# Performance work log

Hardware: AMD Instinct MI355X
Metric: run time of the kernel (lower is better)

The kernel has to match this reference:

```python
import jax, jax.numpy as jnp
import numpy as np

D_MODEL = 1024
D_FF = 4096
NUM_EXPERTS = 8
TOP_K = 2
LN_EPS = 1e-5


def setup_inputs() -> dict:
    key = jax.random.key(0)
    ks = jax.random.split(key, 8)
    B, S = 4, 2048
    x = jax.random.normal(ks[0], (B, S, D_MODEL), dtype=jnp.float32)
    router_w = jax.random.normal(ks[1], (D_MODEL, NUM_EXPERTS), dtype=jnp.float32) * (1.0 / np.sqrt(D_MODEL))
    router_b = jnp.zeros((NUM_EXPERTS,), dtype=jnp.float32)
    w1 = jax.random.normal(ks[2], (NUM_EXPERTS, D_MODEL, D_FF), dtype=jnp.float32) * (1.0 / np.sqrt(D_MODEL))
    b1 = jnp.zeros((NUM_EXPERTS, D_FF), dtype=jnp.float32)
    w2 = jax.random.normal(ks[3], (NUM_EXPERTS, D_FF, D_MODEL), dtype=jnp.float32) * (1.0 / np.sqrt(D_FF))
    b2 = jnp.zeros((NUM_EXPERTS, D_MODEL), dtype=jnp.float32)
    gamma = jnp.ones((D_MODEL,), dtype=jnp.float32)
    beta = jnp.zeros((D_MODEL,), dtype=jnp.float32)
    return {"x": x, "router_w": router_w, "router_b": router_b,
            "w1": w1, "b1": b1, "w2": w2, "b2": b2,
            "gamma": gamma, "beta": beta}


def reference(x, router_w, router_b, w1, b1, w2, b2, gamma, beta):
    B, S, D = x.shape
    E = w1.shape[0]
    xf = x.reshape(B * S, D)  # [T, D]

    # Router: linear -> softmax -> top-k (scores are softmax probs of selected experts)
    logits = xf @ router_w + router_b                     # [T, E]
    probs = jax.nn.softmax(logits, axis=-1)
    scores, idx = jax.lax.top_k(probs, TOP_K)             # [T, K]

    # Dense combine weights: comb[t, e] = sum_k scores[t,k] * (idx[t,k]==e)
    comb = (jax.nn.one_hot(idx, E, dtype=x.dtype) * scores[..., None]).sum(axis=1)  # [T, E]

    # Dispatch/compute/combine. comb is 0 for unrouted (token, expert) pairs,
    # so the weighted sum matches the gather/scatter loop in the original.
    out = jnp.zeros_like(xf)
    for e in range(E):  # fixed small expert count, structurally distinct weights
        h = jax.nn.gelu(xf @ w1[e] + b1[e])               # [T, D_FF]
        out = out + comb[:, e:e + 1] * (h @ w2[e] + b2[e])
    out = out.reshape(B, S, D)

    # residual + LayerNorm (dropout = 0.0)
    y = x + out
    mu = y.mean(axis=-1, keepdims=True)
    var = ((y - mu) ** 2).mean(axis=-1, keepdims=True)
    z = (y - mu) * jax.lax.rsqrt(var + LN_EPS) * gamma + beta

    # routing decision export (bool mask over experts, jit-friendly stand-in for a Python set)
    selected = comb.sum(axis=0) > 0
    return z, selected
```

## Files before the change

### kernel.cpp

```cpp
#include <hip/hip_runtime.h>


#define T_TOKENS 8192
#define DM 1024
#define DF 4096
#define NE 8

typedef unsigned short u16;
typedef short v8s __attribute__((ext_vector_type(8)));
typedef float v4f __attribute__((ext_vector_type(4)));

__device__ __forceinline__ u16 f2bf(float f) {
  unsigned u = __float_as_uint(f);
  u += 0x7FFFu + ((u >> 16) & 1u);
  return (u16)(u >> 16);
}

__device__ __forceinline__ void load16_lds(const u16* g, u16* lds) {
  __builtin_amdgcn_global_load_lds(
      (const __attribute__((address_space(1))) unsigned int*)g,
      (__attribute__((address_space(3))) unsigned int*)lds, 16, 0, 0);
}

__global__ __launch_bounds__(256) void cvt_x_kernel(const float* __restrict__ x,
                                                    u16* __restrict__ xb) {
  size_t i = ((size_t)blockIdx.x * 256 + threadIdx.x) * 8;
  float4 v0 = *(const float4*)(x + i);
  float4 v1 = *(const float4*)(x + i + 4);
  int4 o;
  o.x = (int)f2bf(v0.x) | ((int)f2bf(v0.y) << 16);
  o.y = (int)f2bf(v0.z) | ((int)f2bf(v0.w) << 16);
  o.z = (int)f2bf(v1.x) | ((int)f2bf(v1.y) << 16);
  o.w = (int)f2bf(v1.z) | ((int)f2bf(v1.w) << 16);
  *(int4*)(xb + i) = o;
}

__global__ __launch_bounds__(64) void router_kernel(
    const float* __restrict__ x, const float* __restrict__ rw,
    const float* __restrict__ rb, int* __restrict__ counts,
    int* __restrict__ list_token, int* __restrict__ epos,
    float* __restrict__ escore) {
  int t = blockIdx.x;
  int lane = threadIdx.x;
  const float* xr = x + (size_t)t * DM;
  float a[8] = {0.f, 0.f, 0.f, 0.f, 0.f, 0.f, 0.f, 0.f};
  for (int j = lane; j < DM; j += 64) {
    float xv = xr[j];
    const float4* r4 = (const float4*)(rw + (size_t)j * 8);
    float4 w0 = r4[0], w1 = r4[1];
    a[0] += xv * w0.x; a[1] += xv * w0.y; a[2] += xv * w0.z; a[3] += xv * w0.w;
    a[4] += xv * w1.x; a[5] += xv * w1.y; a[6] += xv * w1.z; a[7] += xv * w1.w;
  }
#pragma unroll
  for (int e = 0; e < 8; e++)
#pragma unroll
    for (int off = 32; off > 0; off >>= 1) a[e] += __shfl_down(a[e], off);
  if (lane == 0) {
    float l[8];
    float mx = -1e30f;
#pragma unroll
    for (int e = 0; e < 8; e++) { l[e] = a[e] + rb[e]; mx = fmaxf(mx, l[e]); }
    float sum = 0.f;
#pragma unroll
    for (int e = 0; e < 8; e++) { l[e] = __expf(l[e] - mx); sum += l[e]; }
    float inv = 1.f / sum;
    int i1 = 0; float p1 = -1.f;
#pragma unroll
    for (int e = 0; e < 8; e++) if (l[e] > p1) { p1 = l[e]; i1 = e; }
    int i2 = -1; float p2 = -1.f;
#pragma unroll
    for (int e = 0; e < 8; e++) if (e != i1 && l[e] > p2) { p2 = l[e]; i2 = e; }
    int pos1 = atomicAdd(&counts[i1], 1);
    int pos2 = atomicAdd(&counts[i2], 1);
    list_token[i1 * T_TOKENS + pos1] = t;
    list_token[i2 * T_TOKENS + pos2] = t;
    epos[2 * t] = (i1 << 16) | pos1;
    epos[2 * t + 1] = (i2 << 16) | pos2;
    escore[2 * t] = p1 * inv;
    escore[2 * t + 1] = p2 * inv;
  }
}

__global__ __launch_bounds__(64) void finalize_kernel(const int* __restrict__ counts,
                                                      int* __restrict__ offsets,
                                                      float* __restrict__ sel_out) {
  int tid = threadIdx.x;
  if (tid == 0) {
    int o = 0;
    for (int e = 0; e < NE; e++) { offsets[e] = o; o += counts[e]; }
    offsets[NE] = o;
  }
  if (tid < NE) sel_out[tid] = counts[tid] > 0 ? 1.f : 0.f;
}

__global__ __launch_bounds__(256) void transpose_cvt_kernel(
    const float* __restrict__ src, u16* __restrict__ dst, int R, int C) {
  __shared__ float tile[64][33];
  int e = blockIdx.z;
  const float* s = src + (size_t)e * R * C;
  u16* d = dst + (size_t)e * R * C;
  int c0 = blockIdx.x * 32, r0 = blockIdx.y * 64;
  int tx = threadIdx.x, ty = threadIdx.y;
#pragma unroll
  for (int i = 0; i < 8; i++) {
    int r = r0 + ty + i * 8;
    tile[ty + i * 8][tx] = s[(size_t)r * C + c0 + tx];
  }
  __syncthreads();
#pragma unroll
  for (int i = 0; i < 4; i++) {
    int c = c0 + ty + i * 8;
    unsigned lo = f2bf(tile[2 * tx][ty + i * 8]);
    unsigned hi = f2bf(tile[2 * tx + 1][ty + i * 8]);
    *(unsigned*)&d[(size_t)c * R + r0 + 2 * tx] = lo | (hi << 16);
  }
}

__global__ __launch_bounds__(256) void gemm1_kernel(
    const u16* __restrict__ xb, const u16* __restrict__ w1t,
    const float* __restrict__ b1, const int* __restrict__ counts,
    const int* __restrict__ offsets, const int* __restrict__ list_token,
    u16* __restrict__ H) {
  int e = blockIdx.z;
  int cnt = counts[e];
  int r0 = blockIdx.y * 128;
  if (r0 >= cnt) return;
  int n0 = blockIdx.x * 128;
  int rem = cnt - r0;

  __shared__ __align__(16) u16 As[128 * 32];
  __shared__ __align__(16) u16 Bs[128 * 32];

  int tid = threadIdx.x;
  int ra0 = tid >> 2, ca0 = tid & 3;
  int ra1 = ra0 + 64, ca1 = ca0;
  const int* lst = list_token + e * T_TOKENS + r0;
  int tok0 = (ra0 < rem) ? lst[ra0] : lst[0];
  int tok1 = (ra1 < rem) ? lst[ra1] : lst[0];
  const u16* gA0 = xb + (size_t)tok0 * DM + ca0 * 8;
  const u16* gA1 = xb + (size_t)tok1 * DM + ca1 * 8;
  const u16* gB0 = w1t + ((size_t)e * DF + n0 + ra0) * DM + ca0 * 8;
  const u16* gB1 = w1t + ((size_t)e * DF + n0 + ra1) * DM + ca1 * 8;

  int lane = tid & 63, wv = tid >> 6;
  u16* ldsA0 = As + wv * 512;
  u16* ldsA1 = As + 2048 + wv * 512;
  u16* ldsB0 = Bs + wv * 512;
  u16* ldsB1 = Bs + 2048 + wv * 512;

  int wm = (wv >> 1) * 64, wn = (wv & 1) * 64;
  int ml = lane & 15, quad = lane >> 4;

  v4f acc[4][4];
#pragma unroll
  for (int i = 0; i < 4; i++)
#pragma unroll
    for (int j = 0; j < 4; j++) acc[i][j] = (v4f){0.f, 0.f, 0.f, 0.f};

  for (int k0 = 0; k0 < DM; k0 += 32) {
    load16_lds(gA0 + k0, ldsA0);
    load16_lds(gA1 + k0, ldsA1);
    load16_lds(gB0 + k0, ldsB0);
    load16_lds(gB1 + k0, ldsB1);
    __syncthreads();
    v8s af[4], bf[4];
#pragma unroll
    for (int i = 0; i < 4; i++)
      af[i] = *(const v8s*)&As[(wm + i * 16 + ml) * 32 + quad * 8];
#pragma unroll
    for (int j = 0; j < 4; j++)
      bf[j] = *(const v8s*)&Bs[(wn + j * 16 + ml) * 32 + quad * 8];
#pragma unroll
    for (int i = 0; i < 4; i++)
#pragma unroll
      for (int j = 0; j < 4; j++)
        acc[i][j] = __builtin_amdgcn_mfma_f32_16x16x32_bf16(af[i], bf[j], acc[i][j], 0, 0, 0);
    __syncthreads();
  }

  int slotbase = offsets[e] + r0;
#pragma unroll
  for (int i = 0; i < 4; i++) {
    int rbase = wm + i * 16 + quad * 4;
#pragma unroll
    for (int j = 0; j < 4; j++) {
      int cc = n0 + wn + j * 16 + ml;
      float bias = b1[e * DF + cc];
#pragma unroll
      for (int r = 0; r < 4; r++) {
        int row = rbase + r;
        if (row < rem) {
          float v = acc[i][j][r] + bias;
          float u = 0.7978845608028654f * (v + 0.044715f * v * v * v);
          float h = v / (1.f + __expf(-2.f * u));
          H[(size_t)(slotbase + row) * DF + cc] = f2bf(h);
        }
      }
    }
  }
}

__global__ __launch_bounds__(256) void gemm2_kernel(
    const u16* __restrict__ H, const u16* __restrict__ w2t,
    const float* __restrict__ b2, const int* __restrict__ counts,
    const int* __restrict__ offsets, float* __restrict__ partial) {
  int e = blockIdx.z;
  int cnt = counts[e];
  int r0 = blockIdx.y * 128;
  if (r0 >= cnt) return;
  int n0 = blockIdx.x * 128;
  int rem = cnt - r0;
  int slotbase = offsets[e] + r0;

  __shared__ __align__(16) u16 As[128 * 32];
  __shared__ __align__(16) u16 Bs[128 * 32];

  int tid = threadIdx.x;
  int ra0 = tid >> 2, ca0 = tid & 3;
  int ra1 = ra0 + 64, ca1 = ca0;
  int ar0 = (ra0 < rem) ? ra0 : 0;
  int ar1 = (ra1 < rem) ? ra1 : 0;
  const u16* gA0 = H + (size_t)(slotbase + ar0) * DF + ca0 * 8;
  const u16* gA1 = H + (size_t)(slotbase + ar1) * DF + ca1 * 8;
  const u16* gB0 = w2t + ((size_t)e * DM + n0 + ra0) * DF + ca0 * 8;
  const u16* gB1 = w2t + ((size_t)e * DM + n0 + ra1) * DF + ca1 * 8;

  int lane = tid & 63, wv = tid >> 6;
  u16* ldsA0 = As + wv * 512;
  u16* ldsA1 = As + 2048 + wv * 512;
  u16* ldsB0 = Bs + wv * 512;
  u16* ldsB1 = Bs + 2048 + wv * 512;

  int wm = (wv >> 1) * 64, wn = (wv & 1) * 64;
  int ml = lane & 15, quad = lane >> 4;

  v4f acc[4][4];
#pragma unroll
  for (int i = 0; i < 4; i++)
#pragma unroll
    for (int j = 0; j < 4; j++) acc[i][j] = (v4f){0.f, 0.f, 0.f, 0.f};

  for (int k0 = 0; k0 < DF; k0 += 32) {
    load16_lds(gA0 + k0, ldsA0);
    load16_lds(gA1 + k0, ldsA1);
    load16_lds(gB0 + k0, ldsB0);
    load16_lds(gB1 + k0, ldsB1);
    __syncthreads();
    v8s af[4], bf[4];
#pragma unroll
    for (int i = 0; i < 4; i++)
      af[i] = *(const v8s*)&As[(wm + i * 16 + ml) * 32 + quad * 8];
#pragma unroll
    for (int j = 0; j < 4; j++)
      bf[j] = *(const v8s*)&Bs[(wn + j * 16 + ml) * 32 + quad * 8];
#pragma unroll
    for (int i = 0; i < 4; i++)
#pragma unroll
      for (int j = 0; j < 4; j++)
        acc[i][j] = __builtin_amdgcn_mfma_f32_16x16x32_bf16(af[i], bf[j], acc[i][j], 0, 0, 0);
    __syncthreads();
  }

#pragma unroll
  for (int i = 0; i < 4; i++) {
    int rbase = wm + i * 16 + quad * 4;
#pragma unroll
    for (int j = 0; j < 4; j++) {
      int cc = n0 + wn + j * 16 + ml;
      float bias = b2[e * DM + cc];
#pragma unroll
      for (int r = 0; r < 4; r++) {
        int row = rbase + r;
        if (row < rem)
          partial[(size_t)(slotbase + row) * DM + cc] = acc[i][j][r] + bias;
      }
    }
  }
}

__global__ __launch_bounds__(256) void ln_kernel(
    const float* __restrict__ x, const float* __restrict__ partial,
    const int* __restrict__ offsets, const int* __restrict__ epos,
    const float* __restrict__ escore, const float* __restrict__ gamma,
    const float* __restrict__ beta, float* __restrict__ out) {
  int t = blockIdx.x;
  int tid = threadIdx.x;
  int e0p = epos[2 * t], e1p = epos[2 * t + 1];
  float s0 = escore[2 * t], s1 = escore[2 * t + 1];
  size_t row0 = (size_t)offsets[e0p >> 16] + (e0p & 0xFFFF);
  size_t row1 = (size_t)offsets[e1p >> 16] + (e1p & 0xFFFF);
  float4 xv = ((const float4*)(x + (size_t)t * DM))[tid];
  float4 p0 = ((const float4*)(partial + row0 * DM))[tid];
  float4 p1 = ((const float4*)(partial + row1 * DM))[tid];
  float4 y;
  y.x = xv.x + s0 * p0.x + s1 * p1.x;
  y.y = xv.y + s0 * p0.y + s1 * p1.y;
  y.z = xv.z + s0 * p0.z + s1 * p1.z;
  y.w = xv.w + s0 * p0.w + s1 * p1.w;
  float s = y.x + y.y + y.z + y.w;
  float ss = y.x * y.x + y.y * y.y + y.z * y.z + y.w * y.w;
#pragma unroll
  for (int off = 32; off > 0; off >>= 1) {
    s += __shfl_down(s, off);
    ss += __shfl_down(ss, off);
  }
  __shared__ float red[10];
  int wid = tid >> 6, lane = tid & 63;
  if (lane == 0) { red[wid] = s; red[4 + wid] = ss; }
  __syncthreads();
  if (tid == 0) {
    float S = red[0] + red[1] + red[2] + red[3];
    float SS = red[4] + red[5] + red[6] + red[7];
    float mu = S * (1.f / DM);
    float var = SS * (1.f / DM) - mu * mu;
    red[8] = mu;
    red[9] = rsqrtf(var + 1e-5f);
  }
  __syncthreads();
  float mu = red[8], rs = red[9];
  float4 g = ((const float4*)gamma)[tid];
  float4 b = ((const float4*)beta)[tid];
  float4 z;
  z.x = (y.x - mu) * rs * g.x + b.x;
  z.y = (y.y - mu) * rs * g.y + b.y;
  z.z = (y.z - mu) * rs * g.z + b.z;
  z.w = (y.w - mu) * rs * g.w + b.w;
  ((float4*)(out + (size_t)t * DM))[tid] = z;
}

extern "C" void kernel_launch(void* const* d_in, const int* in_sizes, int n_in,
                              void* d_out, int out_size, void* d_ws, size_t ws_size,
                              hipStream_t stream) {
  const float* x = (const float*)d_in[0];
  const float* rw = (const float*)d_in[1];
  const float* rb = (const float*)d_in[2];
  const float* w1 = (const float*)d_in[3];
  const float* b1 = (const float*)d_in[4];
  const float* w2 = (const float*)d_in[5];
  const float* b2 = (const float*)d_in[6];
  const float* gamma = (const float*)d_in[7];
  const float* beta = (const float*)d_in[8];
  float* out = (float*)d_out;

  char* ws = (char*)d_ws;
  int* counts = (int*)(ws + 0);
  int* offsets = (int*)(ws + 256);
  int* list_token = (int*)(ws + 4096);
  int* epos = (int*)(ws + 266240);
  float* escore = (float*)(ws + 331776);
  u16* xb = (u16*)(ws + 1048576);
  u16* w1t = (u16*)(ws + 17825792);
  u16* w2t = (u16*)(ws + 84934656);
  u16* H = (u16*)(ws + 152043520);
  float* partial = (float*)(ws + 286261248);

  hipMemsetAsync(counts, 0, NE * sizeof(int), stream);

  cvt_x_kernel<<<dim3(4096), dim3(256), 0, stream>>>(x, xb);
  router_kernel<<<dim3(T_TOKENS), dim3(64), 0, stream>>>(x, rw, rb, counts,
                                                         list_token, epos, escore);
  finalize_kernel<<<dim3(1), dim3(64), 0, stream>>>(
      counts, offsets, out + (size_t)T_TOKENS * DM);
  transpose_cvt_kernel<<<dim3(128, 16, NE), dim3(32, 8), 0, stream>>>(w1, w1t, DM, DF);
  transpose_cvt_kernel<<<dim3(32, 64, NE), dim3(32, 8), 0, stream>>>(w2, w2t, DF, DM);

  gemm1_kernel<<<dim3(DF / 128, 64, NE), dim3(256), 0, stream>>>(
      xb, w1t, b1, counts, offsets, list_token, H);
  gemm2_kernel<<<dim3(DM / 128, 64, NE), dim3(256), 0, stream>>>(
      H, w2t, b2, counts, offsets, partial);
  ln_kernel<<<dim3(T_TOKENS), dim3(256), 0, stream>>>(x, partial, offsets, epos,
                                                      escore, gamma, beta, out);
}
```

Measured before the change: 1.034 ms.

## Fuse x conversion into router, widen transpose tiles, pack GELU output stores

Drops the separate x-to-bf16 kernel and has the router write the bf16 copy while it reads x, with the router now running four tokens per 256-thread block. The weight transpose-convert kernel moves to 64x64 tiles with float4 loads and 16-byte packed bf16 stores. gemm1's epilogue exchanges neighbouring columns through a lane shuffle so each even lane writes two bf16 values as one 32-bit store. These changes aim to cut launch overhead and memory transactions in the preprocessing and epilogue stages. The router's bf16 stores are 2-byte scalar writes, and the shuffle must now run on every lane, including rows past the valid count.

```diff
diff --git a/kernel.cpp b/kernel.cpp
--- a/kernel.cpp
+++ b/kernel.cpp
@@ -22,30 +22,19 @@
       (__attribute__((address_space(3))) unsigned int*)lds, 16, 0, 0);
 }
 
-__global__ __launch_bounds__(256) void cvt_x_kernel(const float* __restrict__ x,
-                                                    u16* __restrict__ xb) {
-  size_t i = ((size_t)blockIdx.x * 256 + threadIdx.x) * 8;
-  float4 v0 = *(const float4*)(x + i);
-  float4 v1 = *(const float4*)(x + i + 4);
-  int4 o;
-  o.x = (int)f2bf(v0.x) | ((int)f2bf(v0.y) << 16);
-  o.y = (int)f2bf(v0.z) | ((int)f2bf(v0.w) << 16);
-  o.z = (int)f2bf(v1.x) | ((int)f2bf(v1.y) << 16);
-  o.w = (int)f2bf(v1.z) | ((int)f2bf(v1.w) << 16);
-  *(int4*)(xb + i) = o;
-}
-
-__global__ __launch_bounds__(64) void router_kernel(
+__global__ __launch_bounds__(256) void router_kernel(
     const float* __restrict__ x, const float* __restrict__ rw,
     const float* __restrict__ rb, int* __restrict__ counts,
     int* __restrict__ list_token, int* __restrict__ epos,
-    float* __restrict__ escore) {
-  int t = blockIdx.x;
-  int lane = threadIdx.x;
+    float* __restrict__ escore, u16* __restrict__ xb) {
+  int w = threadIdx.x >> 6, lane = threadIdx.x & 63;
+  int t = blockIdx.x * 4 + w;
   const float* xr = x + (size_t)t * DM;
+  u16* xbr = xb + (size_t)t * DM;
   float a[8] = {0.f, 0.f, 0.f, 0.f, 0.f, 0.f, 0.f, 0.f};
   for (int j = lane; j < DM; j += 64) {
     float xv = xr[j];
+    xbr[j] = f2bf(xv);
     const float4* r4 = (const float4*)(rw + (size_t)j * 8);
     float4 w0 = r4[0], w1 = r4[1];
     a[0] += xv * w0.x; a[1] += xv * w0.y; a[2] += xv * w0.z; a[3] += xv * w0.w;
@@ -95,24 +84,36 @@
 
 __global__ __launch_bounds__(256) void transpose_cvt_kernel(
     const float* __restrict__ src, u16* __restrict__ dst, int R, int C) {
-  __shared__ float tile[64][33];
+  __shared__ float tile[64 * 65];
   int e = blockIdx.z;
   const float* s = src + (size_t)e * R * C;
   u16* d = dst + (size_t)e * R * C;
-  int c0 = blockIdx.x * 32, r0 = blockIdx.y * 64;
-  int tx = threadIdx.x, ty = threadIdx.y;
-#pragma unroll
-  for (int i = 0; i < 8; i++) {
-    int r = r0 + ty + i * 8;
-    tile[ty + i * 8][tx] = s[(size_t)r * C + c0 + tx];
+  int r0 = blockIdx.y * 64, c0 = blockIdx.x * 64;
+  int tid = threadIdx.x;
+  int pr = tid >> 4, pc4 = (tid & 15) * 4;
+#pragma unroll
+  for (int i = 0; i < 4; i++) {
+    int r = pr + i * 16;
+    float4 v = *(const float4*)(s + (size_t)(r0 + r) * C + c0 + pc4);
+    tile[r * 65 + pc4] = v.x;
+    tile[r * 65 + pc4 + 1] = v.y;
+    tile[r * 65 + pc4 + 2] = v.z;
+    tile[r * 65 + pc4 + 3] = v.w;
   }
   __syncthreads();
-#pragma unroll
-  for (int i = 0; i < 4; i++) {
-    int c = c0 + ty + i * 8;
-    unsigned lo = f2bf(tile[2 * tx][ty + i * 8]);
-    unsigned hi = f2bf(tile[2 * tx + 1][ty + i * 8]);
-    *(unsigned*)&d[(size_t)c * R + r0 + 2 * tx] = lo | (hi << 16);
+  int r8 = (tid & 7) * 8, cb = tid >> 3;
+#pragma unroll
+  for (int i = 0; i < 2; i++) {
+    int c = cb + i * 32;
+    unsigned pk0 = (unsigned)f2bf(tile[(r8 + 0) * 65 + c]) |
+                   ((unsigned)f2bf(tile[(r8 + 1) * 65 + c]) << 16);
+    unsigned pk1 = (unsigned)f2bf(tile[(r8 + 2) * 65 + c]) |
+                   ((unsigned)f2bf(tile[(r8 + 3) * 65 + c]) << 16);
+    unsigned pk2 = (unsigned)f2bf(tile[(r8 + 4) * 65 + c]) |
+                   ((unsigned)f2bf(tile[(r8 + 5) * 65 + c]) << 16);
+    unsigned pk3 = (unsigned)f2bf(tile[(r8 + 6) * 65 + c]) |
+                   ((unsigned)f2bf(tile[(r8 + 7) * 65 + c]) << 16);
+    *(uint4*)(d + (size_t)(c0 + c) * R + r0 + r8) = make_uint4(pk0, pk1, pk2, pk3);
   }
 }
 
@@ -133,14 +134,14 @@
 
   int tid = threadIdx.x;
   int ra0 = tid >> 2, ca0 = tid & 3;
-  int ra1 = ra0 + 64, ca1 = ca0;
+  int ra1 = ra0 + 64;
   const int* lst = list_token + e * T_TOKENS + r0;
   int tok0 = (ra0 < rem) ? lst[ra0] : lst[0];
   int tok1 = (ra1 < rem) ? lst[ra1] : lst[0];
   const u16* gA0 = xb + (size_t)tok0 * DM + ca0 * 8;
-  const u16* gA1 = xb + (size_t)tok1 * DM + ca1 * 8;
+  const u16* gA1 = xb + (size_t)tok1 * DM + ca0 * 8;
   const u16* gB0 = w1t + ((size_t)e * DF + n0 + ra0) * DM + ca0 * 8;
-  const u16* gB1 = w1t + ((size_t)e * DF + n0 + ra1) * DM + ca1 * 8;
+  const u16* gB1 = w1t + ((size_t)e * DF + n0 + ra1) * DM + ca0 * 8;
 
   int lane = tid & 63, wv = tid >> 6;
   u16* ldsA0 = As + wv * 512;
@@ -189,11 +190,13 @@
 #pragma unroll
       for (int r = 0; r < 4; r++) {
         int row = rbase + r;
-        if (row < rem) {
-          float v = acc[i][j][r] + bias;
-          float u = 0.7978845608028654f * (v + 0.044715f * v * v * v);
-          float h = v / (1.f + __expf(-2.f * u));
-          H[(size_t)(slotbase + row) * DF + cc] = f2bf(h);
+        float v = acc[i][j][r] + bias;
+        float u = 0.7978845608028654f * (v + 0.044715f * v * v * v);
+        float h = v / (1.f + __expf(-2.f * u));
+        float hp = __shfl_xor(h, 1);
+        if (((ml & 1) == 0) && row < rem) {
+          unsigned pk = (unsigned)f2bf(h) | ((unsigned)f2bf(hp) << 16);
+          *(unsigned*)&H[(size_t)(slotbase + row) * DF + cc] = pk;
         }
       }
     }
@@ -217,13 +220,13 @@
 
   int tid = threadIdx.x;
   int ra0 = tid >> 2, ca0 = tid & 3;
-  int ra1 = ra0 + 64, ca1 = ca0;
+  int ra1 = ra0 + 64;
   int ar0 = (ra0 < rem) ? ra0 : 0;
   int ar1 = (ra1 < rem) ? ra1 : 0;
   const u16* gA0 = H + (size_t)(slotbase + ar0) * DF + ca0 * 8;
-  const u16* gA1 = H + (size_t)(slotbase + ar1) * DF + ca1 * 8;
+  const u16* gA1 = H + (size_t)(slotbase + ar1) * DF + ca0 * 8;
   const u16* gB0 = w2t + ((size_t)e * DM + n0 + ra0) * DF + ca0 * 8;
-  const u16* gB1 = w2t + ((size_t)e * DM + n0 + ra1) * DF + ca1 * 8;
+  const u16* gB1 = w2t + ((size_t)e * DM + n0 + ra1) * DF + ca0 * 8;
 
   int lane = tid & 63, wv = tid >> 6;
   u16* ldsA0 = As + wv * 512;
@@ -356,13 +359,12 @@
 
   hipMemsetAsync(counts, 0, NE * sizeof(int), stream);
 
-  cvt_x_kernel<<<dim3(4096), dim3(256), 0, stream>>>(x, xb);
-  router_kernel<<<dim3(T_TOKENS), dim3(64), 0, stream>>>(x, rw, rb, counts,
-                                                         list_token, epos, escore);
+  router_kernel<<<dim3(T_TOKENS / 4), dim3(256), 0, stream>>>(
+      x, rw, rb, counts, list_token, epos, escore, xb);
   finalize_kernel<<<dim3(1), dim3(64), 0, stream>>>(
       counts, offsets, out + (size_t)T_TOKENS * DM);
-  transpose_cvt_kernel<<<dim3(128, 16, NE), dim3(32, 8), 0, stream>>>(w1, w1t, DM, DF);
-  transpose_cvt_kernel<<<dim3(32, 64, NE), dim3(32, 8), 0, stream>>>(w2, w2t, DF, DM);
+  transpose_cvt_kernel<<<dim3(64, 16, NE), dim3(256), 0, stream>>>(w1, w1t, DM, DF);
+  transpose_cvt_kernel<<<dim3(16, 64, NE), dim3(256), 0, stream>>>(w2, w2t, DF, DM);
 
   gemm1_kernel<<<dim3(DF / 128, 64, NE), dim3(256), 0, stream>>>(
       xb, w1t, b1, counts, offsets, list_token, H);
```

Measured after the change: 1.010 ms. 2.3% less time.
